# Optimization experiments

Hardware: AMD Instinct MI355X
Metric: run time of the kernel (lower is better)

Reference implementation:

```python
import jax, jax.numpy as jnp
import numpy as np

EMBED = 768
HEADS = 12
HEAD_DIM = EMBED // HEADS
NUM_BUCKETS = 32
MAX_DISTANCE = 128


def _relative_buckets(tgt_len, src_len):
    ctx = jnp.arange(tgt_len)[:, None]
    mem = jnp.arange(src_len)[None, :]
    rel = mem - ctx                                  # [T, S]
    nb = NUM_BUCKETS // 2                            # 16
    buckets = (rel > 0).astype(jnp.int32) * nb
    rp = jnp.abs(rel)
    max_exact = nb // 2                              # 8
    is_small = rp < max_exact
    rp_safe = jnp.maximum(rp, 1).astype(jnp.float32)
    large = max_exact + (
        jnp.log(rp_safe / max_exact) / np.log(MAX_DISTANCE / max_exact) * (nb - max_exact)
    ).astype(jnp.int32)
    large = jnp.minimum(large, nb - 1)
    buckets = buckets + jnp.where(is_small, rp, large)
    return buckets                                   # [T, S] int32


def setup_inputs() -> dict:
    key = jax.random.key(0)
    ks = jax.random.split(key, 12)
    T, B, E = 2048, 2, EMBED
    def xavier(k, shape, gain=1.0):
        fan_in, fan_out = shape[0], shape[1]
        a = gain * np.sqrt(6.0 / (fan_in + fan_out))
        return jax.random.uniform(k, shape, jnp.float32, -a, a)
    g = 1.0 / np.sqrt(2.0)
    return {
        "query": jax.random.normal(ks[0], (T, B, E), jnp.float32),
        "key": jax.random.normal(ks[1], (T, B, E), jnp.float32),
        "value": jax.random.normal(ks[2], (T, B, E), jnp.float32),
        "key_padding_mask": jnp.zeros((B, T), dtype=bool),
        # weights stored [in, out] (transpose of torch Linear)
        "Wq": xavier(ks[3], (E, E), g), "bq": jnp.zeros((E,), jnp.float32),
        "Wk": xavier(ks[4], (E, E), g), "bk": jnp.zeros((E,), jnp.float32),
        "Wv": xavier(ks[5], (E, E), g), "bv": jnp.zeros((E,), jnp.float32),
        "Wo": xavier(ks[6], (E, E), 1.0), "bo": jnp.zeros((E,), jnp.float32),
        "rel_bias": jax.random.normal(ks[7], (NUM_BUCKETS, HEADS), jnp.float32)
        * np.sqrt(2.0 / (NUM_BUCKETS + HEADS)),
    }


def reference(query, key, value, key_padding_mask, Wq, bq, Wk, bk, Wv, bv, Wo, bo, rel_bias):
    T, B, E = query.shape
    S = key.shape[0]
    scaling = HEAD_DIM ** -0.5
    q = (query @ Wq + bq) * scaling
    k = key @ Wk + bk
    v = value @ Wv + bv
    # [T,B,E] -> [B,H,T,D]
    def split_heads(x, L):
        return x.reshape(L, B, HEADS, HEAD_DIM).transpose(1, 2, 0, 3)
    qh, kh, vh = split_heads(q, T), split_heads(k, S), split_heads(v, S)
    # T5 relative position bias: [H, T, S]
    buckets = _relative_buckets(T, S)
    position_bias = rel_bias[buckets].transpose(2, 0, 1)  # [H,T,S]
    scores = jnp.einsum("bhtd,bhsd->bhts", qh, kh) + position_bias[None]
    scores = jnp.where(key_padding_mask[:, None, None, :], -jnp.inf, scores)
    probs = jax.nn.softmax(scores, axis=-1)
    attn = jnp.einsum("bhts,bhsd->bhtd", probs, vh)
    attn = attn.transpose(2, 0, 1, 3).reshape(T, B, E)
    return attn @ Wo + bo
```

## Files before the change

### kernel.cpp

```cpp
#include <hip/hip_runtime.h>
#include <hip/hip_bf16.h>

typedef __bf16 bf16;
typedef __bf16 bf16x8 __attribute__((ext_vector_type(8)));
typedef float f32x4 __attribute__((ext_vector_type(4)));

#define EMB 768
#define NH 12
#define HD 64
#define SEQ 2048
#define NBATCH 2
#define NREL (2 * SEQ - 1)
#define LOG2E 1.44269504088896f

__device__ __forceinline__ int swz(int bo) { return bo ^ ((bo >> 3) & 0x70); }
__device__ __forceinline__ int swz256(int bo) { return bo ^ ((bo >> 4) & 0x70); }
__device__ __forceinline__ int kpos(int s) {
  return (s & 0x23) | ((s & 0x04) << 2) | ((s & 0x18) >> 1);
}
__device__ __forceinline__ float fexp2(float x) {
  return __builtin_amdgcn_exp2f(x);
}

typedef __attribute__((address_space(3))) unsigned int lds_u32;
typedef __attribute__((address_space(1))) unsigned int glb_u32;
__device__ __forceinline__ void gld16(const void* g, void* l) {
  __builtin_amdgcn_global_load_lds((const glb_u32*)g, (lds_u32*)l, 16, 0, 0);
}

__global__ __launch_bounds__(256) void k_setup(
    const float* __restrict__ Xq, const float* __restrict__ Xk,
    const float* __restrict__ Xv, const float* __restrict__ Wq,
    const float* __restrict__ Wk, const float* __restrict__ Wv,
    const float* __restrict__ Wo, const unsigned char* __restrict__ mask,
    const float* __restrict__ rel_bias, bf16* __restrict__ ximg,
    bf16* __restrict__ wimg, float* __restrict__ bias_tab,
    unsigned long long* __restrict__ mbits) {
  __shared__ __align__(16) bf16 T[64 * 128];
  const int idx = blockIdx.x;
  const int tid = threadIdx.x;
  if (idx < 1152) {
    const int z = idx / 384, rem = idx % 384;
    const int mb = rem % 32, ks = rem / 32;
    const float* X = z == 0 ? Xq : z == 1 ? Xk : Xv;
    const int m0 = mb * 128, k0 = ks * 64;
    char* img = (char*)ximg + ((size_t)(z * 32 + mb) * 12 + ks) * 16384;
#pragma unroll
    for (int it = 0; it < 4; ++it) {
      int i = tid + it * 256;
      int mr = i >> 3, kc8 = (i & 7) * 8;
      const float* xp = X + (size_t)(m0 + mr) * EMB + k0 + kc8;
      float4 f0 = *(const float4*)xp, f1 = *(const float4*)(xp + 4);
      bf16x8 hh;
      hh[0] = (bf16)f0.x; hh[1] = (bf16)f0.y; hh[2] = (bf16)f0.z; hh[3] = (bf16)f0.w;
      hh[4] = (bf16)f1.x; hh[5] = (bf16)f1.y; hh[6] = (bf16)f1.z; hh[7] = (bf16)f1.w;
      *(bf16x8*)(img + swz(mr * 128 + kc8 * 2)) = hh;
    }
  } else if (idx < 1440) {
    const int i = idx - 1152;
    const int z = i / 72, rem = i % 72;
    const int nb = rem % 6, ks = rem / 6;
    const float* W = z == 0 ? Wq : z == 1 ? Wk : z == 2 ? Wv : Wo;
    const int n0 = nb * 128, k0 = ks * 64;
    {
      int kk = tid >> 2, nn0 = (tid & 3) * 32;
      const float* wp = W + (size_t)(k0 + kk) * EMB + n0 + nn0;
#pragma unroll
      for (int jq = 0; jq < 4; ++jq) {
        float4 f0 = *(const float4*)(wp + jq * 8);
        float4 f1 = *(const float4*)(wp + jq * 8 + 4);
        bf16x8 hh;
        hh[0] = (bf16)f0.x; hh[1] = (bf16)f0.y; hh[2] = (bf16)f0.z; hh[3] = (bf16)f0.w;
        hh[4] = (bf16)f1.x; hh[5] = (bf16)f1.y; hh[6] = (bf16)f1.z; hh[7] = (bf16)f1.w;
        *(bf16x8*)((char*)T + swz256(kk * 256 + (nn0 + jq * 8) * 2)) = hh;
      }
    }
    __syncthreads();
    {
      int nr = tid >> 1, kh = tid & 1;
      char* img = (char*)wimg + ((size_t)(z * 6 + nb) * 12 + ks) * 16384;
#pragma unroll
      for (int jq = 0; jq < 4; ++jq) {
        union { bf16 e[8]; uint4 u; } pk;
#pragma unroll
        for (int q = 0; q < 8; ++q)
          pk.e[q] = *(const bf16*)((char*)T + swz256((kh * 32 + jq * 8 + q) * 256 + nr * 2));
        *(uint4*)(img + swz(nr * 128 + (kh * 32 + jq * 8) * 2)) = pk.u;
      }
    }
  } else if (idx < 1456) {
    int i = (idx - 1440) * 256 + tid;
    if (i < NREL) {
      int rel = i - (SEQ - 1);
      int bkt = (rel > 0) ? 16 : 0;
      int rp = rel < 0 ? -rel : rel;
      if (rp < 8) {
        bkt += rp;
      } else {
        float lf = (logf((float)rp * 0.125f) / 2.7725887222397811f) * 8.0f;
        int large = 8 + (int)lf;
        bkt += (large < 15) ? large : 15;
      }
      for (int h = 0; h < NH; ++h)
        bias_tab[h * NREL + i] = rel_bias[bkt * NH + h] * LOG2E;
    }
  } else {
    int wid = (idx - 1456) * 4 + (tid >> 6);
    int lane = tid & 63;
    int b = wid >> 5, wd = wid & 31;
    unsigned long long m = __ballot(mask[b * SEQ + wd * 64 + lane] != 0);
    if (lane == 0) mbits[wid] = m;
  }
}

__global__ __launch_bounds__(256) void k_proj_qkv(
    const bf16* __restrict__ ximg, const bf16* __restrict__ wimg,
    const float* __restrict__ bq, const float* __restrict__ bk,
    const float* __restrict__ bv, bf16* __restrict__ oq,
    bf16* __restrict__ gk, bf16* __restrict__ gv) {
  __shared__ __align__(16) bf16 AB[2][2][8192];
  const int z = blockIdx.z;
  const float* bias = z == 0 ? bq : z == 1 ? bk : bv;
  const float scale = z == 0 ? 0.125f * LOG2E : 1.0f;
  const int mb = blockIdx.x, nb = blockIdx.y;
  const int m0 = mb * 128, n0 = nb * 128;
  const int tid = threadIdx.x, lane = tid & 63, w = tid >> 6;
  const int c = lane & 15, g = lane >> 4;
  const int mo = (w >> 1) * 64, no = (w & 1) * 64;
  const char* abase = (const char*)ximg + (size_t)(z * 32 + mb) * 12 * 16384;
  const char* bbase = (const char*)wimg + (size_t)(z * 6 + nb) * 12 * 16384;

#define PISSUE(KS, BUF) do {                                               \
    const char* a_ = abase + (size_t)(KS) * 16384;                         \
    const char* b_ = bbase + (size_t)(KS) * 16384;                         \
    _Pragma("unroll") for (int ch = 0; ch < 4; ++ch) {                     \
      int ck = w * 4 + ch;                                                 \
      gld16(a_ + ck * 1024 + lane * 16, (char*)AB[BUF][0] + ck * 1024);    \
      gld16(b_ + ck * 1024 + lane * 16, (char*)AB[BUF][1] + ck * 1024);    \
    }                                                                      \
  } while (0)

  PISSUE(0, 0);
  f32x4 acc[4][4] = {};
  asm volatile("s_waitcnt vmcnt(0)" ::: "memory");
  __syncthreads();
  for (int ks = 0; ks < 12; ++ks) {
    const int cur = ks & 1;
    if (ks < 11) PISSUE(ks + 1, cur ^ 1);
    const char* As = (const char*)AB[cur][0];
    const char* Bs = (const char*)AB[cur][1];
    __builtin_amdgcn_s_setprio(1);
#pragma unroll
    for (int kk = 0; kk < 2; ++kk) {
      bf16x8 av[4], bvf[4];
#pragma unroll
      for (int mf = 0; mf < 4; ++mf)
        av[mf] = *(const bf16x8*)(As + swz((mo + mf * 16 + c) * 128 + kk * 64 + g * 16));
#pragma unroll
      for (int nf = 0; nf < 4; ++nf)
        bvf[nf] = *(const bf16x8*)(Bs + swz((no + nf * 16 + c) * 128 + kk * 64 + g * 16));
#pragma unroll
      for (int mf = 0; mf < 4; ++mf)
#pragma unroll
        for (int nf = 0; nf < 4; ++nf)
          acc[mf][nf] = __builtin_amdgcn_mfma_f32_16x16x32_bf16(bvf[nf], av[mf], acc[mf][nf], 0, 0, 0);
    }
    __builtin_amdgcn_s_setprio(0);
    if (ks < 11) {
      asm volatile("s_waitcnt vmcnt(0)" ::: "memory");
      __syncthreads();
    }
  }
#pragma unroll
  for (int nf = 0; nf < 4; ++nf) {
    int n = n0 + no + nf * 16 + g * 4;
    float4 b4 = *(const float4*)&bias[n];
#pragma unroll
    for (int mf = 0; mf < 4; ++mf) {
      int m = m0 + mo + mf * 16 + c;
      float v0 = (acc[mf][nf][0] + b4.x) * scale;
      float v1 = (acc[mf][nf][1] + b4.y) * scale;
      float v2 = (acc[mf][nf][2] + b4.z) * scale;
      float v3 = (acc[mf][nf][3] + b4.w) * scale;
      if (z == 0) {
        union { bf16 e[4]; uint2 u; } pk;
        pk.e[0] = (bf16)v0; pk.e[1] = (bf16)v1; pk.e[2] = (bf16)v2; pk.e[3] = (bf16)v3;
        *(uint2*)(oq + (size_t)m * EMB + n) = pk.u;
      } else if (z == 1) {
        int t = m >> 1, bb = m & 1;
        int hh = n >> 6, d = n & 63;
        union { bf16 e[4]; uint2 u; } pk;
        pk.e[0] = (bf16)v0; pk.e[1] = (bf16)v1; pk.e[2] = (bf16)v2; pk.e[3] = (bf16)v3;
        char* base = (char*)gk + ((size_t)(bb * NH + hh) * 32 + (t >> 6)) * 8192;
        *(uint2*)(base + swz(kpos(t & 63) * 128 + (d & ~7) * 2) + (d & 4) * 2) = pk.u;
      } else {
        int s = m >> 1, bb = m & 1;
        int hh = n >> 6, d0 = n & 63;
        char* base = (char*)gv + ((size_t)(bb * NH + hh) * 32 + (s >> 6)) * 8192;
        int sc2 = (s & 63) * 2;
        *(bf16*)(base + (((d0 + 0) * 128 + sc2) ^ (((d0 + 0) & 7) << 4))) = (bf16)v0;
        *(bf16*)(base + (((d0 + 1) * 128 + sc2) ^ (((d0 + 1) & 7) << 4))) = (bf16)v1;
        *(bf16*)(base + (((d0 + 2) * 128 + sc2) ^ (((d0 + 2) & 7) << 4))) = (bf16)v2;
        *(bf16*)(base + (((d0 + 3) * 128 + sc2) ^ (((d0 + 3) & 7) << 4))) = (bf16)v3;
      }
    }
  }
#undef PISSUE
}

__global__ __launch_bounds__(256) void k_proj_out(
    const bf16* __restrict__ aimg, const bf16* __restrict__ wimg,
    const float* __restrict__ bias, float* __restrict__ out) {
  __shared__ __align__(16) bf16 AB[2][2][8192];
  const int mb = blockIdx.x, nb = blockIdx.y;
  const int m0 = mb * 128, n0 = nb * 128;
  const int tid = threadIdx.x, lane = tid & 63, w = tid >> 6;
  const int c = lane & 15, g = lane >> 4;
  const int mo = (w >> 1) * 64, no = (w & 1) * 64;
  const char* abase = (const char*)aimg + (size_t)mb * 12 * 16384;
  const char* bbase = (const char*)wimg + (size_t)(3 * 6 + nb) * 12 * 16384;

#define PISSUE(KS, BUF) do {                                               \
    const char* a_ = abase + (size_t)(KS) * 16384;                         \
    const char* b_ = bbase + (size_t)(KS) * 16384;                         \
    _Pragma("unroll") for (int ch = 0; ch < 4; ++ch) {                     \
      int ck = w * 4 + ch;                                                 \
      gld16(a_ + ck * 1024 + lane * 16, (char*)AB[BUF][0] + ck * 1024);    \
      gld16(b_ + ck * 1024 + lane * 16, (char*)AB[BUF][1] + ck * 1024);    \
    }                                                                      \
  } while (0)

  PISSUE(0, 0);
  f32x4 acc[4][4] = {};
  asm volatile("s_waitcnt vmcnt(0)" ::: "memory");
  __syncthreads();
  for (int ks = 0; ks < 12; ++ks) {
    const int cur = ks & 1;
    if (ks < 11) PISSUE(ks + 1, cur ^ 1);
    const char* As = (const char*)AB[cur][0];
    const char* Bs = (const char*)AB[cur][1];
    __builtin_amdgcn_s_setprio(1);
#pragma unroll
    for (int kk = 0; kk < 2; ++kk) {
      bf16x8 av[4], bvf[4];
#pragma unroll
      for (int mf = 0; mf < 4; ++mf)
        av[mf] = *(const bf16x8*)(As + swz((mo + mf * 16 + c) * 128 + kk * 64 + g * 16));
#pragma unroll
      for (int nf = 0; nf < 4; ++nf)
        bvf[nf] = *(const bf16x8*)(Bs + swz((no + nf * 16 + c) * 128 + kk * 64 + g * 16));
#pragma unroll
      for (int mf = 0; mf < 4; ++mf)
#pragma unroll
        for (int nf = 0; nf < 4; ++nf)
          acc[mf][nf] = __builtin_amdgcn_mfma_f32_16x16x32_bf16(bvf[nf], av[mf], acc[mf][nf], 0, 0, 0);
    }
    __builtin_amdgcn_s_setprio(0);
    if (ks < 11) {
      asm volatile("s_waitcnt vmcnt(0)" ::: "memory");
      __syncthreads();
    }
  }
#pragma unroll
  for (int nf = 0; nf < 4; ++nf) {
    int n = n0 + no + nf * 16 + g * 4;
    float4 b4 = *(const float4*)&bias[n];
#pragma unroll
    for (int mf = 0; mf < 4; ++mf) {
      int m = m0 + mo + mf * 16 + c;
      float4 v;
      v.x = acc[mf][nf][0] + b4.x;
      v.y = acc[mf][nf][1] + b4.y;
      v.z = acc[mf][nf][2] + b4.z;
      v.w = acc[mf][nf][3] + b4.w;
      *(float4*)(out + (size_t)m * EMB + n) = v;
    }
  }
#undef PISSUE
}

__global__ __launch_bounds__(256, 4) void k_attn(
    const bf16* __restrict__ qb, const bf16* __restrict__ gk,
    const bf16* __restrict__ gv, const unsigned long long* __restrict__ mbits,
    const float* __restrict__ bias_tab, bf16* __restrict__ aimg) {
  __shared__ __align__(16) bf16 KV[2][2][4096];
  __shared__ float Bslow[384];
  const int bh = blockIdx.x;
  const int b = bh / NH, h = bh % NH;
  const int t0 = blockIdx.y * 64;
  const int tid = threadIdx.x;
  const int lane = tid & 63, w = tid >> 6;
  const int c = lane & 15, g = lane >> 4;
  const float NEGINF = -__builtin_inff();
  const int tl = w * 16 + c;

  const char* kimg = (const char*)gk + (size_t)bh * 32 * 8192;
  const char* vimg = (const char*)gv + (size_t)bh * 32 * 8192;

#define ISSUE(IT, BUF) do {                                                  \
    const char* ks_ = kimg + (size_t)(IT) * 8192;                            \
    const char* vs_ = vimg + (size_t)(IT) * 8192;                            \
    _Pragma("unroll") for (int jj = 0; jj < 2; ++jj) {                       \
      int ch = w * 2 + jj;                                                   \
      gld16(ks_ + ch * 1024 + lane * 16, (char*)KV[BUF][0] + ch * 1024);     \
      gld16(vs_ + ch * 1024 + lane * 16, (char*)KV[BUF][1] + ch * 1024);     \
    }                                                                        \
  } while (0)

  ISSUE(0, 0);
  bf16x8 qf[2];
  {
    const bf16* qp = qb + (size_t)((t0 + tl) * NBATCH + b) * EMB + h * 64 + g * 8;
    qf[0] = *(const bf16x8*)qp;
    qf[1] = *(const bf16x8*)(qp + 32);
  }
  const float* btab = bias_tab + h * NREL + (SEQ - 1);
  for (int j = tid; j < 384; j += 256) Bslow[j] = btab[j - 192];
  const float cpos = btab[SEQ - 1];
  const float cneg = btab[-(SEQ - 1)];

  bf16x8 ones8;
#pragma unroll
  for (int j = 0; j < 8; ++j) ones8[j] = (bf16)1.0f;

  float m_p = -1e30f;
  f32x4 lacc = {0.f, 0.f, 0.f, 0.f};
  f32x4 o[4] = {};

  asm volatile("s_waitcnt vmcnt(0)" ::: "memory");
  __syncthreads();

#pragma unroll 2
  for (int it = 0; it < 32; ++it) {
    const int cur = it & 1;
    if (it < 31) ISSUE(it + 1, cur ^ 1);
    const unsigned long long mb = mbits[b * 32 + it];
    const char* Ks = (const char*)KV[cur][0];
    const char* Vs = (const char*)KV[cur][1];

    f32x4 sacc[4] = {};
    __builtin_amdgcn_s_setprio(1);
#pragma unroll
    for (int kk = 0; kk < 2; ++kk) {
#pragma unroll
      for (int nf = 0; nf < 4; ++nf) {
        bf16x8 kf = *(const bf16x8*)(Ks + swz((nf * 16 + c) * 128 + kk * 64 + g * 16));
        sacc[nf] = __builtin_amdgcn_mfma_f32_16x16x32_bf16(kf, qf[kk], sacc[nf], 0, 0, 0);
      }
    }
    __builtin_amdgcn_s_setprio(0);

    const int s0 = it * 64;
    const int d = s0 - t0;
    const bool slow = (d > -192) && (d < 192);
    const float cb = slow ? 0.f : (d >= 192 ? cpos : cneg);

    if (slow) {
      const int bidx = d - tl + 192;
#pragma unroll
      for (int nf = 0; nf < 4; ++nf) {
        int sb = 32 * (nf >> 1) + g * 8 + (nf & 1) * 4;
#pragma unroll
        for (int r = 0; r < 4; ++r) sacc[nf][r] += Bslow[bidx + sb + r];
      }
    }
    if (mb) {
#pragma unroll
      for (int nf = 0; nf < 4; ++nf) {
        int sb = 32 * (nf >> 1) + g * 8 + (nf & 1) * 4;
#pragma unroll
        for (int r = 0; r < 4; ++r)
          if ((mb >> (sb + r)) & 1) sacc[nf][r] = NEGINF;
      }
    }
    f32x4 mx;
#pragma unroll
    for (int r = 0; r < 4; ++r)
      mx[r] = fmaxf(fmaxf(sacc[0][r], sacc[1][r]), fmaxf(sacc[2][r], sacc[3][r]));
    float pmax = fmaxf(fmaxf(mx[0], mx[1]), fmaxf(mx[2], mx[3]));

    if (!__all(pmax + cb <= m_p + 11.5f)) {
      float rmax = fmaxf(pmax, __shfl_xor(pmax, 16, 64));
      rmax = fmaxf(rmax, __shfl_xor(rmax, 32, 64));
      float rm = rmax + cb;
      float m_new = fmaxf(m_p, rm);
      float scl = fexp2(m_p - m_new);
      m_p = m_new;
#pragma unroll
      for (int r = 0; r < 4; ++r) {
        float so = __shfl(scl, g * 4 + r, 64);
        lacc[r] *= so;
#pragma unroll
        for (int nf2 = 0; nf2 < 4; ++nf2) o[nf2][r] *= so;
      }
    }
    const float msh = m_p - cb;
    bf16x8 pa[2];
#pragma unroll
    for (int kk = 0; kk < 2; ++kk)
#pragma unroll
      for (int j = 0; j < 8; ++j)
        pa[kk][j] = (bf16)fexp2(sacc[2 * kk + (j >> 2)][j & 3] - msh);

    __builtin_amdgcn_s_setprio(1);
    lacc = __builtin_amdgcn_mfma_f32_16x16x32_bf16(pa[0], ones8, lacc, 0, 0, 0);
    lacc = __builtin_amdgcn_mfma_f32_16x16x32_bf16(pa[1], ones8, lacc, 0, 0, 0);
#pragma unroll
    for (int kk = 0; kk < 2; ++kk) {
#pragma unroll
      for (int nf2 = 0; nf2 < 4; ++nf2) {
        bf16x8 vbf = *(const bf16x8*)(Vs + swz((nf2 * 16 + c) * 128 + kk * 64 + g * 16));
        o[nf2] = __builtin_amdgcn_mfma_f32_16x16x32_bf16(pa[kk], vbf, o[nf2], 0, 0, 0);
      }
    }
    __builtin_amdgcn_s_setprio(0);

    if (it < 31) {
      asm volatile("s_waitcnt vmcnt(0)" ::: "memory");
      __syncthreads();
    }
  }
#pragma unroll
  for (int r = 0; r < 4; ++r) {
    float inv = 1.0f / lacc[r];
    int t = t0 + w * 16 + g * 4 + r;
    int m = t * NBATCH + b;
    char* base = (char*)aimg + ((size_t)(m >> 7) * 12 + h) * 16384;
    int mr128 = (m & 127) * 128;
#pragma unroll
    for (int nf2 = 0; nf2 < 4; ++nf2) {
      int dd = nf2 * 16 + c;
      *(bf16*)(base + swz(mr128 + dd * 2)) = (bf16)(o[nf2][r] * inv);
    }
  }
#undef ISSUE
}

extern "C" void kernel_launch(void* const* d_in, const int* in_sizes, int n_in,
                              void* d_out, int out_size, void* d_ws, size_t ws_size,
                              hipStream_t stream) {
  const float* query = (const float*)d_in[0];
  const float* key_ = (const float*)d_in[1];
  const float* value = (const float*)d_in[2];
  const unsigned char* kpm = (const unsigned char*)d_in[3];
  const float* Wq = (const float*)d_in[4];
  const float* bq = (const float*)d_in[5];
  const float* Wk = (const float*)d_in[6];
  const float* bk = (const float*)d_in[7];
  const float* Wv = (const float*)d_in[8];
  const float* bv = (const float*)d_in[9];
  const float* Wo = (const float*)d_in[10];
  const float* bo = (const float*)d_in[11];
  const float* rel_bias = (const float*)d_in[12];
  float* out = (float*)d_out;

  char* ws = (char*)d_ws;
  const size_t SZb = (size_t)SEQ * NBATCH * EMB * sizeof(bf16);
  const size_t WIMG = (size_t)4 * 6 * 12 * 16384;
  bf16* qbb = (bf16*)(ws);
  bf16* gkb = (bf16*)(ws + SZb);
  bf16* gvb = (bf16*)(ws + 2 * SZb);
  bf16* wimg = (bf16*)(ws + 3 * SZb);
  float* bias_tab = (float*)(ws + 3 * SZb + WIMG);
  unsigned long long* mbits =
      (unsigned long long*)(ws + 3 * SZb + WIMG + 196608);
  bf16* ximg = (bf16*)(ws + 3 * SZb + WIMG + 196608 + 512);
  bf16* aimg = ximg;

  k_setup<<<1472, 256, 0, stream>>>(query, key_, value, Wq, Wk, Wv, Wo,
                                    kpm, rel_bias, ximg, wimg, bias_tab, mbits);
  k_proj_qkv<<<dim3(32, 6, 3), 256, 0, stream>>>(
      ximg, wimg, bq, bk, bv, qbb, gkb, gvb);
  k_attn<<<dim3(NBATCH * NH, SEQ / 64), 256, 0, stream>>>(
      qbb, gkb, gvb, mbits, bias_tab, aimg);
  k_proj_out<<<dim3(32, 6), 256, 0, stream>>>(aimg, wimg, bo, out);
}
```

Before: 91.73 us.

## Fuse fp32-to-bf16 activation conversion into QKV projection GEMM A-tile loads

Removes the separate pass in the setup kernel that converted the query/key/value activations to swizzled bf16 tiles. The QKV projection kernel now loads fp32 activations straight into registers, converts them, and writes them to LDS inside its double-buffered loop. This drops one full read and write of the activation images to global memory. In exchange, each activation tile is re-read as fp32 by all 6 N-blocks, which doubles A-side global traffic, and the loop gains register-staged conversion work.

New measurement: 105.4 us. 14.9% more time.

```diff
diff --git a/kernel.cpp b/kernel.cpp
--- a/kernel.cpp
+++ b/kernel.cpp
@@ -29,36 +29,16 @@
 }
 
 __global__ __launch_bounds__(256) void k_setup(
-    const float* __restrict__ Xq, const float* __restrict__ Xk,
-    const float* __restrict__ Xv, const float* __restrict__ Wq,
-    const float* __restrict__ Wk, const float* __restrict__ Wv,
-    const float* __restrict__ Wo, const unsigned char* __restrict__ mask,
-    const float* __restrict__ rel_bias, bf16* __restrict__ ximg,
+    const float* __restrict__ Wq, const float* __restrict__ Wk,
+    const float* __restrict__ Wv, const float* __restrict__ Wo,
+    const unsigned char* __restrict__ mask, const float* __restrict__ rel_bias,
     bf16* __restrict__ wimg, float* __restrict__ bias_tab,
     unsigned long long* __restrict__ mbits) {
   __shared__ __align__(16) bf16 T[64 * 128];
   const int idx = blockIdx.x;
   const int tid = threadIdx.x;
-  if (idx < 1152) {
-    const int z = idx / 384, rem = idx % 384;
-    const int mb = rem % 32, ks = rem / 32;
-    const float* X = z == 0 ? Xq : z == 1 ? Xk : Xv;
-    const int m0 = mb * 128, k0 = ks * 64;
-    char* img = (char*)ximg + ((size_t)(z * 32 + mb) * 12 + ks) * 16384;
-#pragma unroll
-    for (int it = 0; it < 4; ++it) {
-      int i = tid + it * 256;
-      int mr = i >> 3, kc8 = (i & 7) * 8;
-      const float* xp = X + (size_t)(m0 + mr) * EMB + k0 + kc8;
-      float4 f0 = *(const float4*)xp, f1 = *(const float4*)(xp + 4);
-      bf16x8 hh;
-      hh[0] = (bf16)f0.x; hh[1] = (bf16)f0.y; hh[2] = (bf16)f0.z; hh[3] = (bf16)f0.w;
-      hh[4] = (bf16)f1.x; hh[5] = (bf16)f1.y; hh[6] = (bf16)f1.z; hh[7] = (bf16)f1.w;
-      *(bf16x8*)(img + swz(mr * 128 + kc8 * 2)) = hh;
-    }
-  } else if (idx < 1440) {
-    const int i = idx - 1152;
-    const int z = i / 72, rem = i % 72;
+  if (idx < 288) {
+    const int z = idx / 72, rem = idx % 72;
     const int nb = rem % 6, ks = rem / 6;
     const float* W = z == 0 ? Wq : z == 1 ? Wk : z == 2 ? Wv : Wo;
     const int n0 = nb * 128, k0 = ks * 64;
@@ -88,8 +68,8 @@
         *(uint4*)(img + swz(nr * 128 + (kh * 32 + jq * 8) * 2)) = pk.u;
       }
     }
-  } else if (idx < 1456) {
-    int i = (idx - 1440) * 256 + tid;
+  } else if (idx < 304) {
+    int i = (idx - 288) * 256 + tid;
     if (i < NREL) {
       int rel = i - (SEQ - 1);
       int bkt = (rel > 0) ? 16 : 0;
@@ -105,7 +85,7 @@
         bias_tab[h * NREL + i] = rel_bias[bkt * NH + h] * LOG2E;
     }
   } else {
-    int wid = (idx - 1456) * 4 + (tid >> 6);
+    int wid = (idx - 304) * 4 + (tid >> 6);
     int lane = tid & 63;
     int b = wid >> 5, wd = wid & 31;
     unsigned long long m = __ballot(mask[b * SEQ + wd * 64 + lane] != 0);
@@ -114,12 +94,14 @@
 }
 
 __global__ __launch_bounds__(256) void k_proj_qkv(
-    const bf16* __restrict__ ximg, const bf16* __restrict__ wimg,
+    const float* __restrict__ Xq, const float* __restrict__ Xk,
+    const float* __restrict__ Xv, const bf16* __restrict__ wimg,
     const float* __restrict__ bq, const float* __restrict__ bk,
     const float* __restrict__ bv, bf16* __restrict__ oq,
     bf16* __restrict__ gk, bf16* __restrict__ gv) {
   __shared__ __align__(16) bf16 AB[2][2][8192];
   const int z = blockIdx.z;
+  const float* X = z == 0 ? Xq : z == 1 ? Xk : Xv;
   const float* bias = z == 0 ? bq : z == 1 ? bk : bv;
   const float scale = z == 0 ? 0.125f * LOG2E : 1.0f;
   const int mb = blockIdx.x, nb = blockIdx.y;
@@ -127,26 +109,49 @@
   const int tid = threadIdx.x, lane = tid & 63, w = tid >> 6;
   const int c = lane & 15, g = lane >> 4;
   const int mo = (w >> 1) * 64, no = (w & 1) * 64;
-  const char* abase = (const char*)ximg + (size_t)(z * 32 + mb) * 12 * 16384;
   const char* bbase = (const char*)wimg + (size_t)(z * 6 + nb) * 12 * 16384;
-
-#define PISSUE(KS, BUF) do {                                               \
-    const char* a_ = abase + (size_t)(KS) * 16384;                         \
+  const int arow = tid >> 3, akc = (tid & 7) * 8;
+
+  float4 af[4][2];
+#define AISSUE(KS) do {                                                    \
+    const float* xp_ = X + (size_t)(m0 + arow) * EMB + (KS) * 64 + akc;    \
+    _Pragma("unroll") for (int j = 0; j < 4; ++j) {                        \
+      af[j][0] = *(const float4*)(xp_ + (size_t)j * 32 * EMB);             \
+      af[j][1] = *(const float4*)(xp_ + (size_t)j * 32 * EMB + 4);         \
+    }                                                                      \
+  } while (0)
+
+#define AWRITE(BUF) do {                                                   \
+    _Pragma("unroll") for (int j = 0; j < 4; ++j) {                        \
+      bf16x8 hh;                                                           \
+      hh[0] = (bf16)af[j][0].x; hh[1] = (bf16)af[j][0].y;                  \
+      hh[2] = (bf16)af[j][0].z; hh[3] = (bf16)af[j][0].w;                  \
+      hh[4] = (bf16)af[j][1].x; hh[5] = (bf16)af[j][1].y;                  \
+      hh[6] = (bf16)af[j][1].z; hh[7] = (bf16)af[j][1].w;                  \
+      *(bf16x8*)((char*)AB[BUF][0] + swz((arow + j * 32) * 128 + akc * 2)) = hh; \
+    }                                                                      \
+  } while (0)
+
+#define BISSUE(KS, BUF) do {                                               \
     const char* b_ = bbase + (size_t)(KS) * 16384;                         \
     _Pragma("unroll") for (int ch = 0; ch < 4; ++ch) {                     \
       int ck = w * 4 + ch;                                                 \
-      gld16(a_ + ck * 1024 + lane * 16, (char*)AB[BUF][0] + ck * 1024);    \
       gld16(b_ + ck * 1024 + lane * 16, (char*)AB[BUF][1] + ck * 1024);    \
     }                                                                      \
   } while (0)
 
-  PISSUE(0, 0);
+  AISSUE(0);
+  BISSUE(0, 0);
   f32x4 acc[4][4] = {};
   asm volatile("s_waitcnt vmcnt(0)" ::: "memory");
+  AWRITE(0);
   __syncthreads();
   for (int ks = 0; ks < 12; ++ks) {
     const int cur = ks & 1;
-    if (ks < 11) PISSUE(ks + 1, cur ^ 1);
+    if (ks < 11) {
+      AISSUE(ks + 1);
+      BISSUE(ks + 1, cur ^ 1);
+    }
     const char* As = (const char*)AB[cur][0];
     const char* Bs = (const char*)AB[cur][1];
     __builtin_amdgcn_s_setprio(1);
@@ -168,6 +173,7 @@
     __builtin_amdgcn_s_setprio(0);
     if (ks < 11) {
       asm volatile("s_waitcnt vmcnt(0)" ::: "memory");
+      AWRITE(cur ^ 1);
       __syncthreads();
     }
   }
@@ -205,7 +211,9 @@
       }
     }
   }
-#undef PISSUE
+#undef AISSUE
+#undef AWRITE
+#undef BISSUE
 }
 
 __global__ __launch_bounds__(256) void k_proj_out(
@@ -464,13 +472,12 @@
   float* bias_tab = (float*)(ws + 3 * SZb + WIMG);
   unsigned long long* mbits =
       (unsigned long long*)(ws + 3 * SZb + WIMG + 196608);
-  bf16* ximg = (bf16*)(ws + 3 * SZb + WIMG + 196608 + 512);
-  bf16* aimg = ximg;
-
-  k_setup<<<1472, 256, 0, stream>>>(query, key_, value, Wq, Wk, Wv, Wo,
-                                    kpm, rel_bias, ximg, wimg, bias_tab, mbits);
+  bf16* aimg = (bf16*)(ws + 3 * SZb + WIMG + 196608 + 512);
+
+  k_setup<<<320, 256, 0, stream>>>(Wq, Wk, Wv, Wo, kpm, rel_bias,
+                                   wimg, bias_tab, mbits);
   k_proj_qkv<<<dim3(32, 6, 3), 256, 0, stream>>>(
-      ximg, wimg, bq, bk, bv, qbb, gkb, gvb);
+      query, key_, value, wimg, bq, bk, bv, qbb, gkb, gvb);
   k_attn<<<dim3(NBATCH * NH, SEQ / 64), 256, 0, stream>>>(
       qbb, gkb, gvb, mbits, bias_tab, aimg);
   k_proj_out<<<dim3(32, 6), 256, 0, stream>>>(aimg, wimg, bo, out);
```

## Split attention over the key dimension into two halves with a merge kernel

Applied to the files above, without the earlier changes.

The attention kernel now splits the key/value sequence into two halves along a new grid dimension. Each block writes unnormalised fp32 partial outputs plus its running max and row sum to a workspace buffer. A new merge kernel rescales and combines the two partials and writes the bf16 image. This doubles the number of attention blocks (768 to 1536) to improve occupancy across CUs, at the cost of an extra launch and extra global traffic for the fp32 partials.

After: 97.92 us. +6.7%, slower.

```diff
diff --git a/kernel.cpp b/kernel.cpp
--- a/kernel.cpp
+++ b/kernel.cpp
@@ -282,12 +282,14 @@
 __global__ __launch_bounds__(256, 4) void k_attn(
     const bf16* __restrict__ qb, const bf16* __restrict__ gk,
     const bf16* __restrict__ gv, const unsigned long long* __restrict__ mbits,
-    const float* __restrict__ bias_tab, bf16* __restrict__ aimg) {
+    const float* __restrict__ bias_tab, float* __restrict__ obuf,
+    float* __restrict__ mlbuf) {
   __shared__ __align__(16) bf16 KV[2][2][4096];
   __shared__ float Bslow[384];
   const int bh = blockIdx.x;
   const int b = bh / NH, h = bh % NH;
   const int t0 = blockIdx.y * 64;
+  const int sh = blockIdx.z;
   const int tid = threadIdx.x;
   const int lane = tid & 63, w = tid >> 6;
   const int c = lane & 15, g = lane >> 4;
@@ -307,7 +309,7 @@
     }                                                                        \
   } while (0)
 
-  ISSUE(0, 0);
+  ISSUE(sh * 16, 0);
   bf16x8 qf[2];
   {
     const bf16* qp = qb + (size_t)((t0 + tl) * NBATCH + b) * EMB + h * 64 + g * 8;
@@ -331,10 +333,11 @@
   __syncthreads();
 
 #pragma unroll 2
-  for (int it = 0; it < 32; ++it) {
+  for (int it = 0; it < 16; ++it) {
+    const int ita = sh * 16 + it;
     const int cur = it & 1;
-    if (it < 31) ISSUE(it + 1, cur ^ 1);
-    const unsigned long long mb = mbits[b * 32 + it];
+    if (it < 15) ISSUE(ita + 1, cur ^ 1);
+    const unsigned long long mb = mbits[b * 32 + ita];
     const char* Ks = (const char*)KV[cur][0];
     const char* Vs = (const char*)KV[cur][1];
 
@@ -350,7 +353,7 @@
     }
     __builtin_amdgcn_s_setprio(0);
 
-    const int s0 = it * 64;
+    const int s0 = ita * 64;
     const int d = s0 - t0;
     const bool slow = (d > -192) && (d < 192);
     const float cb = slow ? 0.f : (d >= 192 ? cpos : cneg);
@@ -415,25 +418,58 @@
     }
     __builtin_amdgcn_s_setprio(0);
 
-    if (it < 31) {
+    if (it < 15) {
       asm volatile("s_waitcnt vmcnt(0)" ::: "memory");
       __syncthreads();
     }
   }
+  const size_t pidx = ((size_t)(bh * 32 + blockIdx.y) * 2 + sh);
+  float* ob = obuf + pidx * 4096;
+  float* ml = mlbuf + pidx * 128;
+  if (g == 0) ml[w * 16 + c] = m_p;
+  if (c == 0) {
+#pragma unroll
+    for (int r = 0; r < 4; ++r) ml[64 + w * 16 + g * 4 + r] = lacc[r];
+  }
 #pragma unroll
   for (int r = 0; r < 4; ++r) {
-    float inv = 1.0f / lacc[r];
-    int t = t0 + w * 16 + g * 4 + r;
-    int m = t * NBATCH + b;
-    char* base = (char*)aimg + ((size_t)(m >> 7) * 12 + h) * 16384;
-    int mr128 = (m & 127) * 128;
-#pragma unroll
-    for (int nf2 = 0; nf2 < 4; ++nf2) {
-      int dd = nf2 * 16 + c;
-      *(bf16*)(base + swz(mr128 + dd * 2)) = (bf16)(o[nf2][r] * inv);
-    }
+    int trow = w * 16 + g * 4 + r;
+#pragma unroll
+    for (int nf2 = 0; nf2 < 4; ++nf2)
+      ob[trow * 64 + nf2 * 16 + c] = o[nf2][r];
   }
 #undef ISSUE
+}
+
+__global__ __launch_bounds__(256) void k_merge(
+    const float* __restrict__ obuf, const float* __restrict__ mlbuf,
+    bf16* __restrict__ aimg) {
+  const int blk = blockIdx.x;
+  const int bh = blk >> 5, tb = blk & 31;
+  const int b = bh / NH, h = bh % NH;
+  const int tid = threadIdx.x;
+  const int tr = tid >> 2, dq = (tid & 3) * 16;
+  const size_t p0 = (size_t)blk * 2 * 4096, p1 = p0 + 4096;
+  const float* ml0 = mlbuf + (size_t)blk * 2 * 128;
+  const float* ml1 = ml0 + 128;
+  float m0 = ml0[tr], l0 = ml0[64 + tr];
+  float m1 = ml1[tr], l1 = ml1[64 + tr];
+  float M = fmaxf(m0, m1);
+  float a0 = fexp2(m0 - M), a1 = fexp2(m1 - M);
+  float inv = 1.0f / (l0 * a0 + l1 * a1);
+  a0 *= inv; a1 *= inv;
+  int t = tb * 64 + tr;
+  int m = t * NBATCH + b;
+  char* base = (char*)aimg + ((size_t)(m >> 7) * 12 + h) * 16384;
+  int mr128 = (m & 127) * 128;
+  union { bf16 e[16]; uint4 u[2]; } pk;
+#pragma unroll
+  for (int j = 0; j < 16; ++j) {
+    float v = obuf[p0 + tr * 64 + dq + j] * a0 + obuf[p1 + tr * 64 + dq + j] * a1;
+    pk.e[j] = (bf16)v;
+  }
+  *(uint4*)(base + swz(mr128 + dq * 2)) = pk.u[0];
+  *(uint4*)(base + swz(mr128 + (dq + 8) * 2)) = pk.u[1];
 }
 
 extern "C" void kernel_launch(void* const* d_in, const int* in_sizes, int n_in,
@@ -466,12 +502,16 @@
       (unsigned long long*)(ws + 3 * SZb + WIMG + 196608);
   bf16* ximg = (bf16*)(ws + 3 * SZb + WIMG + 196608 + 512);
   bf16* aimg = ximg;
+  char* pws = ws + 3 * SZb + WIMG + 196608 + 512 + (size_t)3 * 32 * 12 * 16384;
+  float* obuf = (float*)pws;
+  float* mlbuf = (float*)(pws + (size_t)768 * 2 * 4096 * 4);
 
   k_setup<<<1472, 256, 0, stream>>>(query, key_, value, Wq, Wk, Wv, Wo,
                                     kpm, rel_bias, ximg, wimg, bias_tab, mbits);
   k_proj_qkv<<<dim3(32, 6, 3), 256, 0, stream>>>(
       ximg, wimg, bq, bk, bv, qbb, gkb, gvb);
-  k_attn<<<dim3(NBATCH * NH, SEQ / 64), 256, 0, stream>>>(
-      qbb, gkb, gvb, mbits, bias_tab, aimg);
+  k_attn<<<dim3(NBATCH * NH, SEQ / 64, 2), 256, 0, stream>>>(
+      qbb, gkb, gvb, mbits, bias_tab, obuf, mlbuf);
+  k_merge<<<NBATCH * NH * 32, 256, 0, stream>>>(obuf, mlbuf, aimg);
   k_proj_out<<<dim3(32, 6), 256, 0, stream>>>(aimg, wimg, bo, out);
 }
```
